# Kernel tuning notes

Hardware: AMD Instinct MI355X
Metric: run time of the kernel (lower is better)

Reference implementation:

```python
import jax, jax.numpy as jnp
import numpy as np

B, N, C, H = 8, 1024, 384, 6
D = C // H
SPAN = C  # att_span = pos_ebd_size = dim (module sets max_relative_positions = dim)
SCALE_FACTOR = 3  # 1 + c2p + p2c


def setup_inputs() -> dict:
    key = jax.random.key(0)
    ks = jax.random.split(key, 10)
    w = lambda k, shp: jax.random.normal(k, shp, jnp.float32) * 0.02
    rel_pos = (jnp.arange(N)[:, None] - jnp.arange(N)[None, :]).astype(jnp.int32)
    return {
        "x": jax.random.normal(ks[0], (B, N, C), jnp.float32),
        "relative_pos": rel_pos,
        "rel_embeddings": jax.random.normal(ks[1], (2 * SPAN, C), jnp.float32) * 0.02,
        "Wq": w(ks[2], (C, C)), "bq": jnp.zeros((C,), jnp.float32),
        "Wk": w(ks[3], (C, C)), "bk": jnp.zeros((C,), jnp.float32),
        "Wv": w(ks[4], (C, C)), "bv": jnp.zeros((C,), jnp.float32),
        "Wpk": w(ks[5], (C, C)), "bpk": jnp.zeros((C,), jnp.float32),
        "Wpq": w(ks[6], (C, C)), "bpq": jnp.zeros((C,), jnp.float32),
        "Wo": w(ks[7], (C, C)), "bo": jnp.zeros((C,), jnp.float32),
    }


def reference(x, relative_pos, rel_embeddings, Wq, bq, Wk, bk, Wv, bv,
              Wpk, bpk, Wpq, bpq, Wo, bo):
    Bx, Nx, Cx = x.shape
    # content projections -> (B, H, N, D)
    q = (x @ Wq + bq).reshape(Bx, Nx, H, D).transpose(0, 2, 1, 3)
    k = (x @ Wk + bk).reshape(Bx, Nx, H, D).transpose(0, 2, 1, 3)
    v = (x @ Wv + bv).reshape(Bx, Nx, H, D).transpose(0, 2, 1, 3)
    scale = jnp.sqrt(jnp.asarray(D * SCALE_FACTOR, jnp.float32))
    attn = jnp.einsum('bhnd,bhmd->bhnm', q, k) / scale  # (B,H,N,N)

    # positional projections of rel_embeddings[0:2*SPAN] -> (H, 2*SPAN, D)
    pos_k = (rel_embeddings @ Wpk + bpk).reshape(2 * SPAN, H, D).transpose(1, 0, 2)
    pos_q = (rel_embeddings @ Wpq + bpq).reshape(2 * SPAN, H, D).transpose(1, 0, 2)

    rp = relative_pos.astype(jnp.int32)
    # content->position: gather columns of q @ pos_k^T by bucketed index
    c2p_pos = jnp.clip(rp + SPAN, 0, 2 * SPAN - 1)  # (N,N)
    c2p = jnp.einsum('bhnd,hpd->bhnp', q, pos_k)    # (B,H,N,2*SPAN)
    c2p = jnp.take_along_axis(
        c2p, jnp.broadcast_to(c2p_pos[None, None], (Bx, H, Nx, Nx)), axis=-1)

    # position->content: gather columns of k @ pos_q^T, then transpose
    p2c_pos = jnp.clip(-rp + SPAN, 0, 2 * SPAN - 1)
    p2c = jnp.einsum('bhnd,hpd->bhnp', k, pos_q)    # (B,H,N,2*SPAN)
    p2c = jnp.take_along_axis(
        p2c, jnp.broadcast_to(p2c_pos[None, None], (Bx, H, Nx, Nx)), axis=-1)
    p2c = jnp.swapaxes(p2c, -1, -2)

    attn = attn + (c2p + p2c) / scale
    probs = jax.nn.softmax(attn, axis=-1)
    out = jnp.einsum('bhnm,bhmd->bhnd', probs, v)
    out = out.transpose(0, 2, 1, 3).reshape(Bx, Nx, Cx)
    return out @ Wo + bo
```

## Files before the change

### kernel.cpp

```cpp
#include <hip/hip_runtime.h>
#include <math.h>

typedef __attribute__((ext_vector_type(8))) short short8;
typedef __attribute__((ext_vector_type(4))) float v4f;
typedef __attribute__((ext_vector_type(4))) unsigned short us4;

#define INV_SCALE 0.07216878364870322f

__device__ __forceinline__ unsigned short f2bf(float f) {
  unsigned u = __builtin_bit_cast(unsigned, f);
  u = (u + 0x7FFFu + ((u >> 16) & 1u)) >> 16;
  return (unsigned short)u;
}
__device__ __forceinline__ float bf2f(unsigned short h) {
  unsigned u = ((unsigned)h) << 16;
  return __builtin_bit_cast(float, u);
}

enum { OM_PLAIN = 0, OM_Q = 1, OM_K = 2, OM_VT = 3, OM_PK = 4, OM_PQ = 5 };

__global__ __launch_bounds__(256) void transpose_w(
    const float* __restrict__ Wq, const float* __restrict__ Wk,
    const float* __restrict__ Wv, const float* __restrict__ Wpk,
    const float* __restrict__ Wpq, const float* __restrict__ Wo,
    unsigned short* __restrict__ Wt) {
  __shared__ unsigned short Ts[64][68];
  const int mat = blockIdx.y;
  const float* W = mat == 0 ? Wq : mat == 1 ? Wk : mat == 2 ? Wv
                 : mat == 3 ? Wpk : mat == 4 ? Wpq : Wo;
  const int tk = (blockIdx.x % 6) * 64, tn = (blockIdx.x / 6) * 64;
  const int t = threadIdx.x;
#pragma unroll
  for (int it = 0; it < 4; ++it) {
    int r = (t >> 4) + it * 16, c = (t & 15) * 4;
    float4 v = *(const float4*)(W + (size_t)(tk + r) * 384 + tn + c);
    us4 p = {f2bf(v.x), f2bf(v.y), f2bf(v.z), f2bf(v.w)};
    *(us4*)&Ts[r][c] = p;
  }
  __syncthreads();
  unsigned short* out = Wt + (size_t)mat * 147456;
#pragma unroll
  for (int it = 0; it < 2; ++it) {
    int n = (t >> 3) + it * 32, kc = (t & 7) * 8;
    unsigned short tmp[8];
#pragma unroll
    for (int j = 0; j < 8; ++j) tmp[j] = Ts[kc + j][n];
    *(short8*)(out + (size_t)(tn + n) * 384 + tk + kc) = *(short8*)tmp;
  }
}

template <typename AT, int OMODE>
__device__ __forceinline__ void pgemm_body(
    const AT* __restrict__ A, const unsigned short* __restrict__ Bt,
    const float* __restrict__ bias, void* __restrict__ out,
    int m0, int n0, float scale, unsigned short (*Bs)[392]) {
  const int t = threadIdx.x;
  const int lane = t & 63, w = t >> 6, li = lane & 15, quad = lane >> 4;

  {
    int r = t >> 2, cq = (t & 3) * 96;
#pragma unroll
    for (int i = 0; i < 12; ++i)
      *(short8*)&Bs[r][cq + i * 8] =
          *(const short8*)(Bt + (size_t)(n0 + r) * 384 + cq + i * 8);
  }
  const int row = m0 + w * 16 + li;
  short8 afr[12];
#pragma unroll
  for (int kk = 0; kk < 12; ++kk) {
    if constexpr (sizeof(AT) == 4) {
      float4 u0 = *(const float4*)((const float*)A + (size_t)row * 384 + kk * 32 + quad * 8);
      float4 u1 = *(const float4*)((const float*)A + (size_t)row * 384 + kk * 32 + quad * 8 + 4);
      short8 v;
      v[0] = (short)f2bf(u0.x); v[1] = (short)f2bf(u0.y);
      v[2] = (short)f2bf(u0.z); v[3] = (short)f2bf(u0.w);
      v[4] = (short)f2bf(u1.x); v[5] = (short)f2bf(u1.y);
      v[6] = (short)f2bf(u1.z); v[7] = (short)f2bf(u1.w);
      afr[kk] = v;
    } else {
      afr[kk] = *(const short8*)((const unsigned short*)A + (size_t)row * 384 + kk * 32 + quad * 8);
    }
  }
  __syncthreads();

  v4f acc[4] = {};
#pragma unroll
  for (int kk = 0; kk < 12; ++kk) {
#pragma unroll
    for (int nt = 0; nt < 4; ++nt) {
      short8 bf = *(const short8*)&Bs[nt * 16 + li][kk * 32 + quad * 8];
      acc[nt] = __builtin_amdgcn_mfma_f32_16x16x32_bf16(afr[kk], bf, acc[nt], 0, 0, 0);
    }
  }

#pragma unroll
  for (int nt = 0; nt < 4; ++nt) {
    int col = n0 + nt * 16 + li;
    float bv = bias[col];
    int h = col >> 6, d = col & 63;
#pragma unroll
    for (int i = 0; i < 4; ++i) {
      int orow = m0 + w * 16 + quad * 4 + i;
      float val = (acc[nt][i] + bv) * scale;
      if constexpr (OMODE == OM_PLAIN) {
        ((float*)out)[(size_t)orow * 384 + col] = val;
      } else if constexpr (OMODE == OM_Q || OMODE == OM_K) {
        int b = orow >> 10, n = orow & 1023;
        ((unsigned short*)out)[((size_t)(b * 6 + h) << 16) + (n << 6) + d] = f2bf(val);
      } else if constexpr (OMODE == OM_VT) {
        int b = orow >> 10, n = orow & 1023;
        ((unsigned short*)out)[((size_t)(b * 6 + h) << 16) + (d << 10) + n] = f2bf(val);
      } else {
        ((unsigned short*)out)[(size_t)h * 49152 + (size_t)orow * 64 + d] = f2bf(val);
      }
    }
  }
}

__global__ __launch_bounds__(256, 3) void proj_all(
    const float* __restrict__ x, const float* __restrict__ re,
    const unsigned short* __restrict__ Wt,
    const float* __restrict__ bq, const float* __restrict__ bk,
    const float* __restrict__ bv, const float* __restrict__ bpk,
    const float* __restrict__ bpq,
    unsigned short* __restrict__ qw, unsigned short* __restrict__ kw,
    unsigned short* __restrict__ vtw, unsigned short* __restrict__ pkw,
    unsigned short* __restrict__ pqw) {
  __shared__ __align__(16) unsigned short Bs[64][392];
  const int which = blockIdx.y / 6;
  const int n0 = (blockIdx.y % 6) * 64;
  const int m0 = blockIdx.x * 64;
  if (which >= 3 && m0 >= 768) return;
  const float* A = which < 3 ? x : re;
  const unsigned short* Bt = Wt + (size_t)which * 147456;
  switch (which) {
    case 0: pgemm_body<float, OM_Q >(A, Bt, bq,  qw,  m0, n0, INV_SCALE, Bs); break;
    case 1: pgemm_body<float, OM_K >(A, Bt, bk,  kw,  m0, n0, 1.f, Bs); break;
    case 2: pgemm_body<float, OM_VT>(A, Bt, bv,  vtw, m0, n0, 1.f, Bs); break;
    case 3: pgemm_body<float, OM_PK>(A, Bt, bpk, pkw, m0, n0, 1.f, Bs); break;
    default: pgemm_body<float, OM_PQ>(A, Bt, bpq, pqw, m0, n0, INV_SCALE, Bs); break;
  }
}

__global__ __launch_bounds__(256, 3) void out_gemm(
    const unsigned short* __restrict__ ao, const unsigned short* __restrict__ Bt,
    const float* __restrict__ bo, float* __restrict__ out) {
  __shared__ __align__(16) unsigned short Bs[64][392];
  pgemm_body<unsigned short, OM_PLAIN>(ao, Bt, bo, out,
                                       blockIdx.x * 64, blockIdx.y * 64, 1.f, Bs);
}

#define ASTR 72

__global__ __launch_bounds__(256, 3) void attn_fused(
    const unsigned short* __restrict__ q, const unsigned short* __restrict__ k,
    const unsigned short* __restrict__ vt, const unsigned short* __restrict__ pk,
    const unsigned short* __restrict__ pq, unsigned short* __restrict__ ao) {
  __shared__ __align__(16) unsigned short band1[128][ASTR];
  __shared__ __align__(16) unsigned short band2[128][ASTR];
  __shared__ __align__(16) unsigned short Ps[64][ASTR];

  const int bh = blockIdx.y;
  const int h = bh % 6, b = bh / 6;
  const int n0 = blockIdx.x * 64;
  const int t = threadIdx.x;
  const int lane = t & 63, w = t >> 6;
  const int li = lane & 15, quad = lane >> 4;

  const unsigned short* qb = q + ((size_t)bh << 16);
  const unsigned short* kb = k + ((size_t)bh << 16);
  const unsigned short* vb = vt + ((size_t)bh << 16);
  const unsigned short* pkh = pk + (size_t)h * 49152;
  const unsigned short* pqh = pq + (size_t)h * 49152;

  short8 aq0 = *(const short8*)(qb + (size_t)(n0 + w * 16 + li) * 64 + quad * 8);
  short8 aq1 = *(const short8*)(qb + (size_t)(n0 + w * 16 + li) * 64 + 32 + quad * 8);

  float l_part[4] = {0.f, 0.f, 0.f, 0.f};
  v4f o[4] = {};

  for (int j0 = 0; j0 < 1024; j0 += 64) {
    __syncthreads();
    {
      const int pb = n0 - j0 - 63 + 384;
      int r = t >> 1, c = (t & 1) * 32;
      int src = pb + r;
      src = src < 0 ? 0 : (src > 767 ? 767 : src);
      const unsigned short* p1 = pkh + (size_t)src * 64 + c;
      const unsigned short* p2 = pqh + (size_t)src * 64 + c;
#pragma unroll
      for (int s = 0; s < 4; ++s) {
        *(short8*)&band1[r][c + s * 8] = *(const short8*)(p1 + s * 8);
        *(short8*)&band2[r][c + s * 8] = *(const short8*)(p2 + s * 8);
      }
    }
    __syncthreads();

    short8 ak0 = *(const short8*)(kb + (size_t)(j0 + w * 16 + li) * 64 + quad * 8);
    short8 ak1 = *(const short8*)(kb + (size_t)(j0 + w * 16 + li) * 64 + 32 + quad * 8);

    v4f t1a[8] = {}, t2a[8] = {};
#pragma unroll
    for (int ct = 0; ct < 8; ++ct) {
      short8 b10 = *(const short8*)&band1[ct * 16 + li][quad * 8];
      short8 b11 = *(const short8*)&band1[ct * 16 + li][32 + quad * 8];
      t1a[ct] = __builtin_amdgcn_mfma_f32_16x16x32_bf16(aq0, b10, t1a[ct], 0, 0, 0);
      t1a[ct] = __builtin_amdgcn_mfma_f32_16x16x32_bf16(aq1, b11, t1a[ct], 0, 0, 0);
      short8 b20 = *(const short8*)&band2[ct * 16 + li][quad * 8];
      short8 b21 = *(const short8*)&band2[ct * 16 + li][32 + quad * 8];
      t2a[ct] = __builtin_amdgcn_mfma_f32_16x16x32_bf16(ak0, b20, t2a[ct], 0, 0, 0);
      t2a[ct] = __builtin_amdgcn_mfma_f32_16x16x32_bf16(ak1, b21, t2a[ct], 0, 0, 0);
    }
    __syncthreads();

#pragma unroll
    for (int ct = 0; ct < 8; ++ct) {
      us4 p1 = {f2bf(t1a[ct][0]), f2bf(t1a[ct][1]), f2bf(t1a[ct][2]), f2bf(t1a[ct][3])};
      us4 p2 = {f2bf(t2a[ct][0]), f2bf(t2a[ct][1]), f2bf(t2a[ct][2]), f2bf(t2a[ct][3])};
      *(us4*)&band1[ct * 16 + li][w * 16 + quad * 4] = p1;
      *(us4*)&band2[ct * 16 + li][w * 16 + quad * 4] = p2;
    }
    v4f sqk[4] = {};
#pragma unroll
    for (int nt = 0; nt < 4; ++nt) {
      short8 b0 = *(const short8*)(kb + (size_t)(j0 + nt * 16 + li) * 64 + quad * 8);
      short8 b1 = *(const short8*)(kb + (size_t)(j0 + nt * 16 + li) * 64 + 32 + quad * 8);
      sqk[nt] = __builtin_amdgcn_mfma_f32_16x16x32_bf16(aq0, b0, sqk[nt], 0, 0, 0);
      sqk[nt] = __builtin_amdgcn_mfma_f32_16x16x32_bf16(aq1, b1, sqk[nt], 0, 0, 0);
    }
    __syncthreads();

#pragma unroll
    for (int nt = 0; nt < 4; ++nt) {
      int jl = nt * 16 + li;
#pragma unroll
      for (int i = 0; i < 4; ++i) {
        int nl = w * 16 + quad * 4 + i;
        int r = nl - jl + 63;
        float s = sqk[nt][i] + bf2f(band1[r][nl]) + bf2f(band2[r][jl]);
        float p = __expf(s);
        l_part[i] += p;
        Ps[nl][jl] = f2bf(p);
      }
    }
#pragma unroll
    for (int kst = 0; kst < 2; ++kst) {
      short8 ap = *(const short8*)&Ps[w * 16 + li][kst * 32 + quad * 8];
#pragma unroll
      for (int nt = 0; nt < 4; ++nt) {
        short8 bv2 = *(const short8*)(vb + (size_t)(nt * 16 + li) * 1024 + j0 + kst * 32 + quad * 8);
        o[nt] = __builtin_amdgcn_mfma_f32_16x16x32_bf16(ap, bv2, o[nt], 0, 0, 0);
      }
    }
  }

#pragma unroll
  for (int i = 0; i < 4; ++i) {
    float l = l_part[i];
    l += __shfl_xor(l, 1);
    l += __shfl_xor(l, 2);
    l += __shfl_xor(l, 4);
    l += __shfl_xor(l, 8);
    float inv_l = 1.f / l;
    int nl = w * 16 + quad * 4 + i;
#pragma unroll
    for (int nt = 0; nt < 4; ++nt)
      ao[((size_t)(b * 1024 + n0 + nl)) * 384 + h * 64 + nt * 16 + li] =
          f2bf(o[nt][i] * inv_l);
  }
}

extern "C" void kernel_launch(void* const* d_in, const int* in_sizes, int n_in,
                              void* d_out, int out_size, void* d_ws,
                              size_t ws_size, hipStream_t stream) {
  const float* x   = (const float*)d_in[0];
  const float* re  = (const float*)d_in[2];
  const float* Wq  = (const float*)d_in[3];
  const float* bq  = (const float*)d_in[4];
  const float* Wk  = (const float*)d_in[5];
  const float* bk  = (const float*)d_in[6];
  const float* Wv  = (const float*)d_in[7];
  const float* bv  = (const float*)d_in[8];
  const float* Wpk = (const float*)d_in[9];
  const float* bpk = (const float*)d_in[10];
  const float* Wpq = (const float*)d_in[11];
  const float* bpq = (const float*)d_in[12];
  const float* Wo  = (const float*)d_in[13];
  const float* bo  = (const float*)d_in[14];
  float* out = (float*)d_out;

  unsigned short* ws = (unsigned short*)d_ws;
  unsigned short* Wt  = ws;
  unsigned short* qw  = Wt + 884736;
  unsigned short* kw  = qw + 3145728;
  unsigned short* vtw = kw + 3145728;
  unsigned short* pkw = vtw + 3145728;
  unsigned short* pqw = pkw + 294912;
  unsigned short* aow = pqw + 294912;

  transpose_w<<<dim3(36, 6), 256, 0, stream>>>(Wq, Wk, Wv, Wpk, Wpq, Wo, Wt);
  proj_all<<<dim3(128, 30), 256, 0, stream>>>(x, re, Wt, bq, bk, bv, bpk, bpq,
                                              qw, kw, vtw, pkw, pqw);
  attn_fused<<<dim3(16, 48), 256, 0, stream>>>(qw, kw, vtw, pkw, pqw, aow);
  out_gemm<<<dim3(128, 6), 256, 0, stream>>>(aow, Wt + 5 * 147456, bo, out);
}
```

Measured before the change: 276.3 us.

## Split attention over key halves with atomic partial accumulation and reduce pass

Splits the key dimension of the fused attention kernel into two halves across a new grid z dimension, so twice as many blocks run. Each block now accumulates unnormalised outputs and row sums into fp32 buffers with atomicAdd, and a new reduce_norm kernel normalises them and writes the bf16 output. The inner tile shrinks from 64 to 32 keys and the occupancy hint rises from 3 to 4 blocks per CU, cutting LDS usage and skipping redundant band rows. In exchange it adds a memset, float atomics, an extra kernel launch and extra global traffic. It also relies on softmax without max-subtraction, which the code before already did.

```diff
diff --git a/kernel.cpp b/kernel.cpp
--- a/kernel.cpp
+++ b/kernel.cpp
@@ -151,18 +151,21 @@
 }
 
 #define ASTR 72
-
-__global__ __launch_bounds__(256, 3) void attn_fused(
+#define PSTR 40
+
+__global__ __launch_bounds__(256, 4) void attn_part(
     const unsigned short* __restrict__ q, const unsigned short* __restrict__ k,
     const unsigned short* __restrict__ vt, const unsigned short* __restrict__ pk,
-    const unsigned short* __restrict__ pq, unsigned short* __restrict__ ao) {
-  __shared__ __align__(16) unsigned short band1[128][ASTR];
-  __shared__ __align__(16) unsigned short band2[128][ASTR];
-  __shared__ __align__(16) unsigned short Ps[64][ASTR];
+    const unsigned short* __restrict__ pq, float* __restrict__ po,
+    float* __restrict__ pl) {
+  __shared__ __align__(16) unsigned short band1[96 * ASTR];
+  __shared__ __align__(16) unsigned short band2[96 * ASTR];
+  __shared__ __align__(16) unsigned short Ps[64 * PSTR];
 
   const int bh = blockIdx.y;
-  const int h = bh % 6, b = bh / 6;
+  const int h = bh % 6;
   const int n0 = blockIdx.x * 64;
+  const int jbase = blockIdx.z * 512;
   const int t = threadIdx.x;
   const int lane = t & 63, w = t >> 6;
   const int li = lane & 15, quad = lane >> 4;
@@ -179,50 +182,61 @@
   float l_part[4] = {0.f, 0.f, 0.f, 0.f};
   v4f o[4] = {};
 
-  for (int j0 = 0; j0 < 1024; j0 += 64) {
+  for (int j0 = jbase; j0 < jbase + 512; j0 += 32) {
     __syncthreads();
-    {
-      const int pb = n0 - j0 - 63 + 384;
+    if (t < 192) {
       int r = t >> 1, c = (t & 1) * 32;
-      int src = pb + r;
+      int src = n0 - j0 - 31 + 384 + r;
       src = src < 0 ? 0 : (src > 767 ? 767 : src);
       const unsigned short* p1 = pkh + (size_t)src * 64 + c;
       const unsigned short* p2 = pqh + (size_t)src * 64 + c;
 #pragma unroll
       for (int s = 0; s < 4; ++s) {
-        *(short8*)&band1[r][c + s * 8] = *(const short8*)(p1 + s * 8);
-        *(short8*)&band2[r][c + s * 8] = *(const short8*)(p2 + s * 8);
+        *(short8*)&band1[r * ASTR + c + s * 8] = *(const short8*)(p1 + s * 8);
+        *(short8*)&band2[r * ASTR + c + s * 8] = *(const short8*)(p2 + s * 8);
       }
     }
     __syncthreads();
 
-    short8 ak0 = *(const short8*)(kb + (size_t)(j0 + w * 16 + li) * 64 + quad * 8);
-    short8 ak1 = *(const short8*)(kb + (size_t)(j0 + w * 16 + li) * 64 + 32 + quad * 8);
-
-    v4f t1a[8] = {}, t2a[8] = {};
-#pragma unroll
-    for (int ct = 0; ct < 8; ++ct) {
-      short8 b10 = *(const short8*)&band1[ct * 16 + li][quad * 8];
-      short8 b11 = *(const short8*)&band1[ct * 16 + li][32 + quad * 8];
-      t1a[ct] = __builtin_amdgcn_mfma_f32_16x16x32_bf16(aq0, b10, t1a[ct], 0, 0, 0);
-      t1a[ct] = __builtin_amdgcn_mfma_f32_16x16x32_bf16(aq1, b11, t1a[ct], 0, 0, 0);
-      short8 b20 = *(const short8*)&band2[ct * 16 + li][quad * 8];
-      short8 b21 = *(const short8*)&band2[ct * 16 + li][32 + quad * 8];
-      t2a[ct] = __builtin_amdgcn_mfma_f32_16x16x32_bf16(ak0, b20, t2a[ct], 0, 0, 0);
-      t2a[ct] = __builtin_amdgcn_mfma_f32_16x16x32_bf16(ak1, b21, t2a[ct], 0, 0, 0);
+    us4 t1p[6];
+#pragma unroll
+    for (int ct = 0; ct < 6; ++ct) {
+      v4f a1 = {};
+      short8 b0 = *(const short8*)&band1[(ct * 16 + li) * ASTR + quad * 8];
+      short8 b1 = *(const short8*)&band1[(ct * 16 + li) * ASTR + 32 + quad * 8];
+      a1 = __builtin_amdgcn_mfma_f32_16x16x32_bf16(aq0, b0, a1, 0, 0, 0);
+      a1 = __builtin_amdgcn_mfma_f32_16x16x32_bf16(aq1, b1, a1, 0, 0, 0);
+      us4 p1 = {f2bf(a1[0]), f2bf(a1[1]), f2bf(a1[2]), f2bf(a1[3])};
+      t1p[ct] = p1;
+    }
+    us4 t2p[6];
+    if (w < 2) {
+      short8 ak0 = *(const short8*)(kb + (size_t)(j0 + w * 16 + li) * 64 + quad * 8);
+      short8 ak1 = *(const short8*)(kb + (size_t)(j0 + w * 16 + li) * 64 + 32 + quad * 8);
+#pragma unroll
+      for (int ct = 0; ct < 6; ++ct) {
+        v4f a2 = {};
+        short8 b0 = *(const short8*)&band2[(ct * 16 + li) * ASTR + quad * 8];
+        short8 b1 = *(const short8*)&band2[(ct * 16 + li) * ASTR + 32 + quad * 8];
+        a2 = __builtin_amdgcn_mfma_f32_16x16x32_bf16(ak0, b0, a2, 0, 0, 0);
+        a2 = __builtin_amdgcn_mfma_f32_16x16x32_bf16(ak1, b1, a2, 0, 0, 0);
+        us4 p2 = {f2bf(a2[0]), f2bf(a2[1]), f2bf(a2[2]), f2bf(a2[3])};
+        t2p[ct] = p2;
+      }
     }
     __syncthreads();
 
 #pragma unroll
-    for (int ct = 0; ct < 8; ++ct) {
-      us4 p1 = {f2bf(t1a[ct][0]), f2bf(t1a[ct][1]), f2bf(t1a[ct][2]), f2bf(t1a[ct][3])};
-      us4 p2 = {f2bf(t2a[ct][0]), f2bf(t2a[ct][1]), f2bf(t2a[ct][2]), f2bf(t2a[ct][3])};
-      *(us4*)&band1[ct * 16 + li][w * 16 + quad * 4] = p1;
-      *(us4*)&band2[ct * 16 + li][w * 16 + quad * 4] = p2;
-    }
-    v4f sqk[4] = {};
-#pragma unroll
-    for (int nt = 0; nt < 4; ++nt) {
+    for (int ct = 0; ct < 6; ++ct)
+      *(us4*)&band1[(ct * 16 + li) * ASTR + w * 16 + quad * 4] = t1p[ct];
+    if (w < 2) {
+#pragma unroll
+      for (int ct = 0; ct < 6; ++ct)
+        *(us4*)&band2[(ct * 16 + li) * ASTR + w * 16 + quad * 4] = t2p[ct];
+    }
+    v4f sqk[2] = {};
+#pragma unroll
+    for (int nt = 0; nt < 2; ++nt) {
       short8 b0 = *(const short8*)(kb + (size_t)(j0 + nt * 16 + li) * 64 + quad * 8);
       short8 b1 = *(const short8*)(kb + (size_t)(j0 + nt * 16 + li) * 64 + 32 + quad * 8);
       sqk[nt] = __builtin_amdgcn_mfma_f32_16x16x32_bf16(aq0, b0, sqk[nt], 0, 0, 0);
@@ -231,26 +245,23 @@
     __syncthreads();
 
 #pragma unroll
-    for (int nt = 0; nt < 4; ++nt) {
+    for (int nt = 0; nt < 2; ++nt) {
       int jl = nt * 16 + li;
 #pragma unroll
       for (int i = 0; i < 4; ++i) {
         int nl = w * 16 + quad * 4 + i;
-        int r = nl - jl + 63;
-        float s = sqk[nt][i] + bf2f(band1[r][nl]) + bf2f(band2[r][jl]);
+        int r = nl - jl + 31;
+        float s = sqk[nt][i] + bf2f(band1[r * ASTR + nl]) + bf2f(band2[r * ASTR + jl]);
         float p = __expf(s);
         l_part[i] += p;
-        Ps[nl][jl] = f2bf(p);
+        Ps[nl * PSTR + jl] = f2bf(p);
       }
     }
-#pragma unroll
-    for (int kst = 0; kst < 2; ++kst) {
-      short8 ap = *(const short8*)&Ps[w * 16 + li][kst * 32 + quad * 8];
-#pragma unroll
-      for (int nt = 0; nt < 4; ++nt) {
-        short8 bv2 = *(const short8*)(vb + (size_t)(nt * 16 + li) * 1024 + j0 + kst * 32 + quad * 8);
-        o[nt] = __builtin_amdgcn_mfma_f32_16x16x32_bf16(ap, bv2, o[nt], 0, 0, 0);
-      }
+    short8 ap = *(const short8*)&Ps[(w * 16 + li) * PSTR + quad * 8];
+#pragma unroll
+    for (int nt = 0; nt < 4; ++nt) {
+      short8 bv2 = *(const short8*)(vb + (size_t)(nt * 16 + li) * 1024 + j0 + quad * 8);
+      o[nt] = __builtin_amdgcn_mfma_f32_16x16x32_bf16(ap, bv2, o[nt], 0, 0, 0);
     }
   }
 
@@ -261,13 +272,25 @@
     l += __shfl_xor(l, 2);
     l += __shfl_xor(l, 4);
     l += __shfl_xor(l, 8);
-    float inv_l = 1.f / l;
     int nl = w * 16 + quad * 4 + i;
+    if (li == 0) atomicAdd(&pl[(bh << 10) + n0 + nl], l);
 #pragma unroll
     for (int nt = 0; nt < 4; ++nt)
-      ao[((size_t)(b * 1024 + n0 + nl)) * 384 + h * 64 + nt * 16 + li] =
-          f2bf(o[nt][i] * inv_l);
-  }
+      atomicAdd(&po[((size_t)((bh << 10) + n0 + nl) << 6) + nt * 16 + li], o[nt][i]);
+  }
+}
+
+__global__ __launch_bounds__(256) void reduce_norm(
+    const float* __restrict__ po, const float* __restrict__ pl,
+    unsigned short* __restrict__ aow) {
+  int idx = blockIdx.x * 256 + threadIdx.x;
+  int bhn = idx >> 4, d4 = (idx & 15) * 4;
+  float4 ov = *(const float4*)(po + ((size_t)bhn << 6) + d4);
+  float inv = 1.f / pl[bhn];
+  int bh = bhn >> 10, n = bhn & 1023;
+  int b = bh / 6, h = bh % 6;
+  us4 r = {f2bf(ov.x * inv), f2bf(ov.y * inv), f2bf(ov.z * inv), f2bf(ov.w * inv)};
+  *(us4*)(aow + ((size_t)(b * 1024 + n)) * 384 + h * 64 + d4) = r;
 }
 
 extern "C" void kernel_launch(void* const* d_in, const int* in_sizes, int n_in,
@@ -297,10 +320,14 @@
   unsigned short* pkw = vtw + 3145728;
   unsigned short* pqw = pkw + 294912;
   unsigned short* aow = pqw + 294912;
-
+  float* po = (float*)(aow + 3145728);
+  float* pl = po + 3145728;
+
+  hipMemsetAsync(po, 0, (3145728 + 49152) * sizeof(float), stream);
   transpose_w<<<dim3(36, 6), 256, 0, stream>>>(Wq, Wk, Wv, Wpk, Wpq, Wo, Wt);
   proj_all<<<dim3(128, 30), 256, 0, stream>>>(x, re, Wt, bq, bk, bv, bpk, bpq,
                                               qw, kw, vtw, pkw, pqw);
-  attn_fused<<<dim3(16, 48), 256, 0, stream>>>(qw, kw, vtw, pkw, pqw, aow);
+  attn_part<<<dim3(16, 48, 2), 256, 0, stream>>>(qw, kw, vtw, pkw, pqw, po, pl);
+  reduce_norm<<<dim3(3072), 256, 0, stream>>>(po, pl, aow);
   out_gemm<<<dim3(128, 6), 256, 0, stream>>>(aow, Wt + 5 * 147456, bo, out);
 }
```

Measured after the change: 315.6 us. 14.2% more time.

## Restructure attention band GEMMs to load fragments directly from global memory

Applied to the files above, without the earlier changes.

The positional band tiles are no longer staged through shared memory. Each wave now loads its own pos_k/pos_q rows, all four k tiles and the v tiles straight into registers. The work split is changed so each wave computes a 32-row slice of the c2p and p2c band products for all query and key tiles, and results are written transposed into smaller LDS buffers. This removes one barrier and the LDS staging pass per iteration and hoists the V loads ahead of use. In exchange it holds many more live registers (q fragments for all tiles, k and v fragments), which may hurt occupancy under the 3-waves launch bound.

```diff
diff --git a/kernel.cpp b/kernel.cpp
--- a/kernel.cpp
+++ b/kernel.cpp
@@ -150,15 +150,13 @@
                                        blockIdx.x * 64, blockIdx.y * 64, 1.f, Bs);
 }
 
-#define ASTR 72
-
 __global__ __launch_bounds__(256, 3) void attn_fused(
     const unsigned short* __restrict__ q, const unsigned short* __restrict__ k,
     const unsigned short* __restrict__ vt, const unsigned short* __restrict__ pk,
     const unsigned short* __restrict__ pq, unsigned short* __restrict__ ao) {
-  __shared__ __align__(16) unsigned short band1[128][ASTR];
-  __shared__ __align__(16) unsigned short band2[128][ASTR];
-  __shared__ __align__(16) unsigned short Ps[64][ASTR];
+  __shared__ __align__(16) unsigned short T1t[128][68];
+  __shared__ __align__(16) unsigned short T2t[128][68];
+  __shared__ __align__(16) unsigned short Ps[64][72];
 
   const int bh = blockIdx.y;
   const int h = bh % 6, b = bh / 6;
@@ -173,71 +171,99 @@
   const unsigned short* pkh = pk + (size_t)h * 49152;
   const unsigned short* pqh = pq + (size_t)h * 49152;
 
-  short8 aq0 = *(const short8*)(qb + (size_t)(n0 + w * 16 + li) * 64 + quad * 8);
-  short8 aq1 = *(const short8*)(qb + (size_t)(n0 + w * 16 + li) * 64 + 32 + quad * 8);
+  short8 qf[4][2];
+#pragma unroll
+  for (int nt = 0; nt < 4; ++nt)
+#pragma unroll
+    for (int kst = 0; kst < 2; ++kst)
+      qf[nt][kst] = *(const short8*)(qb + (size_t)(n0 + nt * 16 + li) * 64 +
+                                     kst * 32 + quad * 8);
 
   float l_part[4] = {0.f, 0.f, 0.f, 0.f};
   v4f o[4] = {};
 
   for (int j0 = 0; j0 < 1024; j0 += 64) {
+    const int pb = n0 - j0 - 63 + 384;
+    short8 b1f[2][2], b2f[2][2];
+#pragma unroll
+    for (int ct = 0; ct < 2; ++ct) {
+      int src = pb + w * 32 + ct * 16 + li;
+      src = src < 0 ? 0 : (src > 767 ? 767 : src);
+#pragma unroll
+      for (int kst = 0; kst < 2; ++kst) {
+        b1f[ct][kst] = *(const short8*)(pkh + (size_t)src * 64 + kst * 32 + quad * 8);
+        b2f[ct][kst] = *(const short8*)(pqh + (size_t)src * 64 + kst * 32 + quad * 8);
+      }
+    }
+    short8 kf[4][2];
+#pragma unroll
+    for (int jt = 0; jt < 4; ++jt)
+#pragma unroll
+      for (int kst = 0; kst < 2; ++kst)
+        kf[jt][kst] = *(const short8*)(kb + (size_t)(j0 + jt * 16 + li) * 64 +
+                                       kst * 32 + quad * 8);
+    short8 vf[4][2];
+#pragma unroll
+    for (int dt = 0; dt < 4; ++dt)
+#pragma unroll
+      for (int kst = 0; kst < 2; ++kst)
+        vf[dt][kst] = *(const short8*)(vb + (size_t)(dt * 16 + li) * 1024 + j0 +
+                                       kst * 32 + quad * 8);
+
+    v4f t1[4][2] = {};
+#pragma unroll
+    for (int nt = 0; nt < 4; ++nt)
+#pragma unroll
+      for (int ct = 0; ct < 2; ++ct)
+#pragma unroll
+        for (int kst = 0; kst < 2; ++kst)
+          t1[nt][ct] = __builtin_amdgcn_mfma_f32_16x16x32_bf16(
+              qf[nt][kst], b1f[ct][kst], t1[nt][ct], 0, 0, 0);
+    v4f t2[2][4] = {};
+#pragma unroll
+    for (int ct = 0; ct < 2; ++ct)
+#pragma unroll
+      for (int jt = 0; jt < 4; ++jt)
+#pragma unroll
+        for (int kst = 0; kst < 2; ++kst)
+          t2[ct][jt] = __builtin_amdgcn_mfma_f32_16x16x32_bf16(
+              b2f[ct][kst], kf[jt][kst], t2[ct][jt], 0, 0, 0);
+    v4f sqk[4] = {};
+#pragma unroll
+    for (int jt = 0; jt < 4; ++jt)
+#pragma unroll
+      for (int kst = 0; kst < 2; ++kst)
+        sqk[jt] = __builtin_amdgcn_mfma_f32_16x16x32_bf16(
+            qf[w][kst], kf[jt][kst], sqk[jt], 0, 0, 0);
+
     __syncthreads();
-    {
-      const int pb = n0 - j0 - 63 + 384;
-      int r = t >> 1, c = (t & 1) * 32;
-      int src = pb + r;
-      src = src < 0 ? 0 : (src > 767 ? 767 : src);
-      const unsigned short* p1 = pkh + (size_t)src * 64 + c;
-      const unsigned short* p2 = pqh + (size_t)src * 64 + c;
-#pragma unroll
-      for (int s = 0; s < 4; ++s) {
-        *(short8*)&band1[r][c + s * 8] = *(const short8*)(p1 + s * 8);
-        *(short8*)&band2[r][c + s * 8] = *(const short8*)(p2 + s * 8);
+
+#pragma unroll
+    for (int nt = 0; nt < 4; ++nt)
+#pragma unroll
+      for (int ct = 0; ct < 2; ++ct) {
+        us4 p4 = {f2bf(t1[nt][ct][0]), f2bf(t1[nt][ct][1]),
+                  f2bf(t1[nt][ct][2]), f2bf(t1[nt][ct][3])};
+        *(us4*)&T1t[w * 32 + ct * 16 + li][nt * 16 + quad * 4] = p4;
       }
-    }
+#pragma unroll
+    for (int ct = 0; ct < 2; ++ct)
+#pragma unroll
+      for (int jt = 0; jt < 4; ++jt)
+#pragma unroll
+        for (int i = 0; i < 4; ++i)
+          T2t[w * 32 + ct * 16 + quad * 4 + i][jt * 16 + li] = f2bf(t2[ct][jt][i]);
+
     __syncthreads();
 
-    short8 ak0 = *(const short8*)(kb + (size_t)(j0 + w * 16 + li) * 64 + quad * 8);
-    short8 ak1 = *(const short8*)(kb + (size_t)(j0 + w * 16 + li) * 64 + 32 + quad * 8);
-
-    v4f t1a[8] = {}, t2a[8] = {};
-#pragma unroll
-    for (int ct = 0; ct < 8; ++ct) {
-      short8 b10 = *(const short8*)&band1[ct * 16 + li][quad * 8];
-      short8 b11 = *(const short8*)&band1[ct * 16 + li][32 + quad * 8];
-      t1a[ct] = __builtin_amdgcn_mfma_f32_16x16x32_bf16(aq0, b10, t1a[ct], 0, 0, 0);
-      t1a[ct] = __builtin_amdgcn_mfma_f32_16x16x32_bf16(aq1, b11, t1a[ct], 0, 0, 0);
-      short8 b20 = *(const short8*)&band2[ct * 16 + li][quad * 8];
-      short8 b21 = *(const short8*)&band2[ct * 16 + li][32 + quad * 8];
-      t2a[ct] = __builtin_amdgcn_mfma_f32_16x16x32_bf16(ak0, b20, t2a[ct], 0, 0, 0);
-      t2a[ct] = __builtin_amdgcn_mfma_f32_16x16x32_bf16(ak1, b21, t2a[ct], 0, 0, 0);
-    }
-    __syncthreads();
-
-#pragma unroll
-    for (int ct = 0; ct < 8; ++ct) {
-      us4 p1 = {f2bf(t1a[ct][0]), f2bf(t1a[ct][1]), f2bf(t1a[ct][2]), f2bf(t1a[ct][3])};
-      us4 p2 = {f2bf(t2a[ct][0]), f2bf(t2a[ct][1]), f2bf(t2a[ct][2]), f2bf(t2a[ct][3])};
-      *(us4*)&band1[ct * 16 + li][w * 16 + quad * 4] = p1;
-      *(us4*)&band2[ct * 16 + li][w * 16 + quad * 4] = p2;
-    }
-    v4f sqk[4] = {};
-#pragma unroll
-    for (int nt = 0; nt < 4; ++nt) {
-      short8 b0 = *(const short8*)(kb + (size_t)(j0 + nt * 16 + li) * 64 + quad * 8);
-      short8 b1 = *(const short8*)(kb + (size_t)(j0 + nt * 16 + li) * 64 + 32 + quad * 8);
-      sqk[nt] = __builtin_amdgcn_mfma_f32_16x16x32_bf16(aq0, b0, sqk[nt], 0, 0, 0);
-      sqk[nt] = __builtin_amdgcn_mfma_f32_16x16x32_bf16(aq1, b1, sqk[nt], 0, 0, 0);
-    }
-    __syncthreads();
-
-#pragma unroll
-    for (int nt = 0; nt < 4; ++nt) {
-      int jl = nt * 16 + li;
+#pragma unroll
+    for (int jt = 0; jt < 4; ++jt) {
+      int jl = jt * 16 + li;
 #pragma unroll
       for (int i = 0; i < 4; ++i) {
         int nl = w * 16 + quad * 4 + i;
         int r = nl - jl + 63;
-        float s = sqk[nt][i] + bf2f(band1[r][nl]) + bf2f(band2[r][jl]);
+        float s = sqk[jt][i] + bf2f(T1t[r][nl]) + bf2f(T2t[r][jl]);
         float p = __expf(s);
         l_part[i] += p;
         Ps[nl][jl] = f2bf(p);
@@ -247,10 +273,8 @@
     for (int kst = 0; kst < 2; ++kst) {
       short8 ap = *(const short8*)&Ps[w * 16 + li][kst * 32 + quad * 8];
 #pragma unroll
-      for (int nt = 0; nt < 4; ++nt) {
-        short8 bv2 = *(const short8*)(vb + (size_t)(nt * 16 + li) * 1024 + j0 + kst * 32 + quad * 8);
-        o[nt] = __builtin_amdgcn_mfma_f32_16x16x32_bf16(ap, bv2, o[nt], 0, 0, 0);
-      }
+      for (int dt = 0; dt < 4; ++dt)
+        o[dt] = __builtin_amdgcn_mfma_f32_16x16x32_bf16(ap, vf[dt][kst], o[dt], 0, 0, 0);
     }
   }
 
@@ -264,9 +288,9 @@
     float inv_l = 1.f / l;
     int nl = w * 16 + quad * 4 + i;
 #pragma unroll
-    for (int nt = 0; nt < 4; ++nt)
-      ao[((size_t)(b * 1024 + n0 + nl)) * 384 + h * 64 + nt * 16 + li] =
-          f2bf(o[nt][i] * inv_l);
+    for (int dt = 0; dt < 4; ++dt)
+      ao[((size_t)(b * 1024 + n0 + nl)) * 384 + h * 64 + dt * 16 + li] =
+          f2bf(o[dt][i] * inv_l);
   }
 }
 
```

Result: slower. 322.3 us (+16.7%).
